# Optimization experiments

Measured on AMD Instinct MI355X. Metric: run time of the kernel, lower is better.

## Reference

```python
import jax, jax.numpy as jnp
import numpy as np

B, N, DIM, HEADS, RED = 8, 1024, 768, 12, 2
CR = DIM // RED  # 384 reduced channel dim
HD = CR // HEADS  # 32 head dim
EPS = 1e-5


def layer_norm(x, g, b):
    mu = jnp.mean(x, axis=-1, keepdims=True)
    var = jnp.var(x, axis=-1, keepdims=True)
    return (x - mu) * jax.lax.rsqrt(var + EPS) * g + b


def setup_inputs() -> dict:
    key = jax.random.key(0)
    ks = jax.random.split(key, 8)
    s_in = 1.0 / np.sqrt(DIM)
    s_cr = 1.0 / np.sqrt(CR)
    return {
        "x": jax.random.normal(ks[0], (B, N, DIM), dtype=jnp.float32),
        "ln0_g": jnp.ones((DIM,), jnp.float32),
        "ln0_b": jnp.zeros((DIM,), jnp.float32),
        "w_proj": jax.random.normal(ks[1], (CR, DIM), jnp.float32) * s_in,  # conv1x1 -> linear
        "b_proj": jnp.zeros((CR,), jnp.float32),
        "ln1_g": jnp.ones((CR,), jnp.float32),
        "ln1_b": jnp.zeros((CR,), jnp.float32),
        "wq": jax.random.normal(ks[2], (CR, CR), jnp.float32) * s_cr,
        "wk": jax.random.normal(ks[3], (CR, CR), jnp.float32) * s_cr,
        "wv": jax.random.normal(ks[4], (CR, CR), jnp.float32) * s_cr,
    }


def attention(y, wq, wk, wv):
    # y: [B, N, CR]; 1x1 conv == linear on channel dim
    def heads(w):
        return (y @ w.T).reshape(B, N, HEADS, HD).transpose(0, 2, 1, 3)  # [B,H,N,D]
    q, k, v = heads(wq), heads(wk), heads(wv)
    scale = HD ** -0.5
    attn = jax.nn.softmax(jnp.einsum("bhnd,bhmd->bhnm", q, k) * scale, axis=-1)
    out = jnp.einsum("bhnm,bhmd->bhnd", attn, v)  # [B,H,N,D]
    return out.transpose(0, 2, 1, 3).reshape(B, N, CR)


def reference(x, ln0_g, ln0_b, w_proj, b_proj, ln1_g, ln1_b, wq, wk, wv):
    h = layer_norm(x, ln0_g, ln0_b) @ w_proj.T + b_proj  # [B,N,CR]
    y = layer_norm(h, ln1_g, ln1_b)
    return h + attention(y, wq, wk, wv)
```

## Files before the change

kernel.cpp:

```cpp
#include <hip/hip_runtime.h>
#include <math.h>

#define BB 8
#define NN 1024
#define DIM 768
#define HEADS 12
#define CR 384
#define HD 32
#define MROWS (BB*NN)
#define EPS 1e-5f
#define SCALE_Q 0.25503486f

typedef __attribute__((ext_vector_type(8))) __bf16 bf16x8;
typedef __attribute__((ext_vector_type(8))) unsigned short u16x8;
typedef __attribute__((ext_vector_type(4))) float f32x4;

__device__ __forceinline__ unsigned short f2bf(float f) {
    unsigned int u = __float_as_uint(f);
    u += 0x7fffu + ((u >> 16) & 1u);
    return (unsigned short)(u >> 16);
}

__device__ __forceinline__ unsigned int packbf2(float lo, float hi) {
    return (unsigned int)f2bf(lo) | ((unsigned int)f2bf(hi) << 16);
}

__device__ __forceinline__ void async_cp16(const unsigned short* g, unsigned short* l) {
    __builtin_amdgcn_global_load_lds(
        (const __attribute__((address_space(1))) unsigned int*)g,
        (__attribute__((address_space(3))) unsigned int*)l, 16, 0, 0);
}

__global__ __launch_bounds__(256) void ln0_cast(
    const float* __restrict__ x,
    const float* __restrict__ g, const float* __restrict__ bt,
    unsigned short* __restrict__ a0,
    const float* __restrict__ wp, const float* __restrict__ wq,
    const float* __restrict__ wk, const float* __restrict__ wv,
    unsigned short* __restrict__ wpo, unsigned short* __restrict__ wqkvo)
{
    const int bx = blockIdx.x;
    const int t = threadIdx.x;
    if (bx >= MROWS) {
        int i = (bx - MROWS) * 256 + t;
        const float* src; unsigned short* dst; int off;
        if (i < 73728) { src = wp; dst = wpo; off = i; }
        else {
            int j = i - 73728;
            int sel = j / 36864; off = j % 36864;
            src = sel == 0 ? wq : (sel == 1 ? wk : wv);
            dst = wqkvo + (size_t)sel * 147456;
        }
        float4 v = ((const float4*)src)[off];
        ((ushort4*)dst)[off] = make_ushort4(f2bf(v.x), f2bf(v.y), f2bf(v.z), f2bf(v.w));
        return;
    }
    const int nv = DIM >> 2;
    const float* a = x + (size_t)bx * DIM;
    float4 val = make_float4(0.f, 0.f, 0.f, 0.f);
    float s = 0.f, ss = 0.f;
    if (t < nv) {
        val = ((const float4*)a)[t];
        s = val.x + val.y + val.z + val.w;
        ss = val.x * val.x + val.y * val.y + val.z * val.z + val.w * val.w;
    }
    for (int off = 32; off; off >>= 1) {
        s  += __shfl_down(s, off, 64);
        ss += __shfl_down(ss, off, 64);
    }
    __shared__ float rS[4], rSS[4];
    __shared__ float sh_mu, sh_rs;
    int lane = t & 63, w = t >> 6;
    if (lane == 0) { rS[w] = s; rSS[w] = ss; }
    __syncthreads();
    if (t == 0) {
        float S = rS[0] + rS[1] + rS[2] + rS[3];
        float SS = rSS[0] + rSS[1] + rSS[2] + rSS[3];
        float m = S / DIM;
        sh_mu = m;
        sh_rs = rsqrtf(SS / DIM - m * m + EPS);
    }
    __syncthreads();
    if (t < nv) {
        float m = sh_mu, r = sh_rs;
        float4 gv = ((const float4*)g)[t];
        float4 bv = ((const float4*)bt)[t];
        ((ushort4*)(a0 + (size_t)bx * DIM))[t] = make_ushort4(
            f2bf((val.x - m) * r * gv.x + bv.x),
            f2bf((val.y - m) * r * gv.y + bv.y),
            f2bf((val.z - m) * r * gv.z + bv.z),
            f2bf((val.w - m) * r * gv.w + bv.w));
    }
}

__global__ __launch_bounds__(128) void ln1_sum(
    const float* __restrict__ h0, const float* __restrict__ h1,
    const float* __restrict__ bias,
    const float* __restrict__ g, const float* __restrict__ bt,
    float* __restrict__ hs, unsigned short* __restrict__ y)
{
    const int row = blockIdx.x;
    const int t = threadIdx.x;
    const int nv = CR >> 2;
    float4 val = make_float4(0.f, 0.f, 0.f, 0.f);
    float s = 0.f, ss = 0.f;
    if (t < nv) {
        float4 v0 = ((const float4*)(h0 + (size_t)row * CR))[t];
        float4 v1 = ((const float4*)(h1 + (size_t)row * CR))[t];
        float4 bv = ((const float4*)bias)[t];
        val = make_float4(v0.x + v1.x + bv.x, v0.y + v1.y + bv.y,
                          v0.z + v1.z + bv.z, v0.w + v1.w + bv.w);
        ((float4*)(hs + (size_t)row * CR))[t] = val;
        s = val.x + val.y + val.z + val.w;
        ss = val.x * val.x + val.y * val.y + val.z * val.z + val.w * val.w;
    }
    for (int off = 32; off; off >>= 1) {
        s  += __shfl_down(s, off, 64);
        ss += __shfl_down(ss, off, 64);
    }
    __shared__ float rS[2], rSS[2];
    __shared__ float sh_mu, sh_rs;
    int lane = t & 63, w = t >> 6;
    if (lane == 0) { rS[w] = s; rSS[w] = ss; }
    __syncthreads();
    if (t == 0) {
        float S = rS[0] + rS[1];
        float SS = rSS[0] + rSS[1];
        float m = S / CR;
        sh_mu = m;
        sh_rs = rsqrtf(SS / CR - m * m + EPS);
    }
    __syncthreads();
    if (t < nv) {
        float m = sh_mu, r = sh_rs;
        float4 gv = ((const float4*)g)[t];
        float4 bv = ((const float4*)bt)[t];
        ((ushort4*)(y + (size_t)row * CR))[t] = make_ushort4(
            f2bf((val.x - m) * r * gv.x + bv.x),
            f2bf((val.y - m) * r * gv.y + bv.y),
            f2bf((val.z - m) * r * gv.z + bv.z),
            f2bf((val.w - m) * r * gv.w + bv.w));
    }
}

template<int KD, int NITER, int MODE>
__global__ __launch_bounds__(256) void gemm_mfma(
    const unsigned short* __restrict__ A,
    const unsigned short* __restrict__ W,
    void* __restrict__ C0, void* __restrict__ C1)
{
    __shared__ unsigned short Asm[2 * 128 * 32];
    __shared__ unsigned short Bsm[2 * 128 * 32];
    const int t = threadIdx.x;
    const int wave = t >> 6, lane = t & 63;
    const int l15 = lane & 15, quad = lane >> 4;
    const int m0 = blockIdx.y * 128;
    const int n0 = blockIdx.x * 128;
    const int koff = blockIdx.z * (NITER * 32);
    const int wm = (wave & 1) * 64, wn = (wave >> 1) * 64;

    const int srow = lane >> 2;
    const int skq  = (lane & 3) * 8;
    const unsigned short* gA = A + (size_t)(m0 + wave * 32 + srow) * KD + koff + skq;
    const unsigned short* gB = W + (size_t)(n0 + wave * 32 + srow) * KD + koff + skq;
    unsigned short* lA = Asm + wave * 1024;
    unsigned short* lB = Bsm + wave * 1024;

    async_cp16(gA, lA);
    async_cp16(gA + (size_t)16 * KD, lA + 512);
    async_cp16(gB, lB);
    async_cp16(gB + (size_t)16 * KD, lB + 512);

    f32x4 acc[4][4];
#pragma unroll
    for (int i = 0; i < 4; i++)
#pragma unroll
        for (int j = 0; j < 4; j++) acc[i][j] = (f32x4){0.f, 0.f, 0.f, 0.f};

    for (int it = 0; it < NITER; it++) {
        __syncthreads();
        const int cur = it & 1;
        if (it + 1 < NITER) {
            const int noff = (cur ^ 1) * 4096;
            async_cp16(gA + (it + 1) * 32, lA + noff);
            async_cp16(gA + (size_t)16 * KD + (it + 1) * 32, lA + noff + 512);
            async_cp16(gB + (it + 1) * 32, lB + noff);
            async_cp16(gB + (size_t)16 * KD + (it + 1) * 32, lB + noff + 512);
        }
        const unsigned short* Ab = Asm + cur * 4096;
        const unsigned short* Bb = Bsm + cur * 4096;
        bf16x8 af[4], bfr[4];
#pragma unroll
        for (int i = 0; i < 4; i++)
            af[i] = *(const bf16x8*)(Ab + (wm + i * 16 + l15) * 32 + quad * 8);
#pragma unroll
        for (int j = 0; j < 4; j++)
            bfr[j] = *(const bf16x8*)(Bb + (wn + j * 16 + l15) * 32 + quad * 8);
#pragma unroll
        for (int i = 0; i < 4; i++)
#pragma unroll
            for (int j = 0; j < 4; j++)
                acc[i][j] = __builtin_amdgcn_mfma_f32_16x16x32_bf16(af[i], bfr[j], acc[i][j], 0, 0, 0);
    }

    if constexpr (MODE == 0) {
        float* C = (float*)C0 + (size_t)blockIdx.z * MROWS * CR;
#pragma unroll
        for (int i = 0; i < 4; i++)
#pragma unroll
            for (int j = 0; j < 4; j++)
#pragma unroll
                for (int reg = 0; reg < 4; reg++) {
                    int row = m0 + wm + i * 16 + quad * 4 + reg;
                    int col = n0 + wn + j * 16 + l15;
                    C[(size_t)row * CR + col] = acc[i][j][reg];
                }
    } else {
        unsigned short* Cqk = (unsigned short*)C0;
        unsigned short* Vt  = (unsigned short*)C1;
#pragma unroll
        for (int i = 0; i < 4; i++)
#pragma unroll
            for (int j = 0; j < 4; j++) {
                const int colbase = n0 + wn + j * 16;
                const int token0 = m0 + wm + i * 16 + quad * 4;
                if (colbase < DIM) {
                    const float sc = (colbase < CR) ? SCALE_Q : 1.f;
#pragma unroll
                    for (int reg = 0; reg < 4; reg++)
                        Cqk[(size_t)(token0 + reg) * DIM + colbase + l15] = f2bf(acc[i][j][reg] * sc);
                } else {
                    const int ch = colbase - DIM + l15;
                    uint2 pk;
                    pk.x = packbf2(acc[i][j][0], acc[i][j][1]);
                    pk.y = packbf2(acc[i][j][2], acc[i][j][3]);
                    *(uint2*)(Vt + (size_t)ch * MROWS + token0) = pk;
                }
            }
    }
}

__global__ __launch_bounds__(256) void attn_mfma(
    const unsigned short* __restrict__ qk,
    const unsigned short* __restrict__ vt,
    const float* __restrict__ h, float* __restrict__ out)
{
    const int qt = blockIdx.x;
    const int bh = blockIdx.y;
    const int b = bh / HEADS, head = bh % HEADS;
    const int hc = head * HD;
    const int t = threadIdx.x;
    const int wave = t >> 6, lane = t & 63;
    const int l15 = lane & 15, quad = lane >> 4;
    const int q0 = qt * 128;

    __shared__ unsigned short Ks[64 * 40];
    __shared__ unsigned short Vs[32 * 72];
    __shared__ unsigned short Ps[4][32 * 72];
    unsigned short* Pw = Ps[wave];

    bf16x8 qa[2];
#pragma unroll
    for (int qi = 0; qi < 2; qi++)
        qa[qi] = *(const bf16x8*)(qk + (size_t)(b * NN + q0 + wave * 32 + qi * 16 + l15) * DIM
                                  + hc + quad * 8);

    const int rr = t >> 2, seg = t & 3;
    const unsigned short* gK = qk + (size_t)(b * NN + rr) * DIM + CR + hc + seg * 8;
    const int vch = wave * 8 + (lane >> 3), vko = (lane & 7) * 8;
    const unsigned short* gV = vt + (size_t)(hc + vch) * MROWS + b * NN + vko;

    u16x8 kreg = *(const u16x8*)gK;
    u16x8 vreg = *(const u16x8*)gV;

    f32x4 o[2][2] = {{{0.f,0.f,0.f,0.f},{0.f,0.f,0.f,0.f}},
                     {{0.f,0.f,0.f,0.f},{0.f,0.f,0.f,0.f}}};
    float lpart[2] = {0.f, 0.f};

    for (int kt = 0; kt < 16; kt++) {
        __syncthreads();
        *(u16x8*)(Ks + rr * 40 + seg * 8) = kreg;
        *(u16x8*)(Vs + vch * 72 + vko) = vreg;
        if (kt < 15) {
            kreg = *(const u16x8*)(gK + (size_t)(kt + 1) * 64 * DIM);
            vreg = *(const u16x8*)(gV + (kt + 1) * 64);
        }
        __syncthreads();

        bf16x8 kb[4];
#pragma unroll
        for (int nt = 0; nt < 4; nt++)
            kb[nt] = *(const bf16x8*)(Ks + (nt * 16 + l15) * 40 + quad * 8);

#pragma unroll
        for (int qi = 0; qi < 2; qi++) {
            f32x4 s[4];
#pragma unroll
            for (int nt = 0; nt < 4; nt++) {
                f32x4 z = {0.f, 0.f, 0.f, 0.f};
                s[nt] = __builtin_amdgcn_mfma_f32_16x16x32_bf16(kb[nt], qa[qi], z, 0, 0, 0);
            }
#pragma unroll
            for (int nt = 0; nt < 4; nt++) {
                float e0 = __builtin_amdgcn_exp2f(s[nt][0]);
                float e1 = __builtin_amdgcn_exp2f(s[nt][1]);
                float e2 = __builtin_amdgcn_exp2f(s[nt][2]);
                float e3 = __builtin_amdgcn_exp2f(s[nt][3]);
                lpart[qi] += (e0 + e1) + (e2 + e3);
                uint2 pk;
                pk.x = packbf2(e0, e1);
                pk.y = packbf2(e2, e3);
                *(uint2*)(Pw + (qi * 16 + l15) * 72 + nt * 16 + quad * 4) = pk;
            }
        }

        bf16x8 vb[2][2];
#pragma unroll
        for (int kk = 0; kk < 2; kk++)
#pragma unroll
            for (int nt2 = 0; nt2 < 2; nt2++)
                vb[kk][nt2] = *(const bf16x8*)(Vs + (nt2 * 16 + l15) * 72 + kk * 32 + quad * 8);

#pragma unroll
        for (int qi = 0; qi < 2; qi++)
#pragma unroll
            for (int kk = 0; kk < 2; kk++) {
                bf16x8 pa = *(const bf16x8*)(Pw + (qi * 16 + l15) * 72 + kk * 32 + quad * 8);
#pragma unroll
                for (int nt2 = 0; nt2 < 2; nt2++)
                    o[qi][nt2] = __builtin_amdgcn_mfma_f32_16x16x32_bf16(pa, vb[kk][nt2], o[qi][nt2], 0, 0, 0);
            }
    }

#pragma unroll
    for (int qi = 0; qi < 2; qi++) {
        float l = lpart[qi];
        l += __shfl_xor(l, 16, 64);
        l += __shfl_xor(l, 32, 64);
        const float linv = 1.f / l;
#pragma unroll
        for (int reg = 0; reg < 4; reg++) {
            const float li = __shfl(linv, quad * 4 + reg, 64);
            const size_t row = (size_t)(b * NN + q0 + wave * 32 + qi * 16 + quad * 4 + reg);
#pragma unroll
            for (int nt2 = 0; nt2 < 2; nt2++) {
                size_t idx = row * CR + hc + nt2 * 16 + l15;
                out[idx] = h[idx] + o[qi][nt2][reg] * li;
            }
        }
    }
}

extern "C" void kernel_launch(void* const* d_in, const int* in_sizes, int n_in,
                              void* d_out, int out_size, void* d_ws, size_t ws_size,
                              hipStream_t stream) {
    const float* x      = (const float*)d_in[0];
    const float* ln0_g  = (const float*)d_in[1];
    const float* ln0_b  = (const float*)d_in[2];
    const float* w_proj = (const float*)d_in[3];
    const float* b_proj = (const float*)d_in[4];
    const float* ln1_g  = (const float*)d_in[5];
    const float* ln1_b  = (const float*)d_in[6];
    const float* wq     = (const float*)d_in[7];
    const float* wk     = (const float*)d_in[8];
    const float* wv     = (const float*)d_in[9];
    float* out = (float*)d_out;

    char* base = (char*)d_ws;
    unsigned short* a0   = (unsigned short*)base;
    unsigned short* qkb  = (unsigned short*)base;
    float*          hp   = (float*)(base + 12582912);
    float*          hbuf = (float*)(base + 37748736);
    unsigned short* yb   = (unsigned short*)(base + 50331648);
    unsigned short* vtb  = (unsigned short*)(base + 56623104);
    unsigned short* wp   = (unsigned short*)(base + 62914560);
    unsigned short* wqkv = (unsigned short*)(base + 63504384);

    ln0_cast<<<MROWS + 720, 256, 0, stream>>>(x, ln0_g, ln0_b, a0,
                                              w_proj, wq, wk, wv, wp, wqkv);
    gemm_mfma<DIM, 12, 0><<<dim3(CR / 128, MROWS / 128, 2), 256, 0, stream>>>(
        a0, wp, hp, nullptr);
    ln1_sum<<<MROWS, 128, 0, stream>>>(hp, hp + (size_t)MROWS * CR, b_proj,
                                       ln1_g, ln1_b, hbuf, yb);
    gemm_mfma<CR, 12, 1><<<dim3(1152 / 128, MROWS / 128, 1), 256, 0, stream>>>(
        yb, wqkv, qkb, vtb);
    attn_mfma<<<dim3(NN / 128, BB * HEADS), 256, 0, stream>>>(qkb, vtb, hbuf, out);
}
```

Measured before the change: 165.3 us.

## Fuse all stages into one persistent cooperative kernel with grid syncs

Replaces the five separate kernel launches with a single persistent cooperative kernel that loops over row, GEMM-tile and attention-tile jobs. Stages are separated by grid-wide barriers instead of kernel boundaries, and the layer norms use one wave per row with shuffle reductions instead of a block per row. The aim is to remove launch gaps and tail effects between stages. In exchange, work is limited to the resident block count (at most 512), grid.sync has its own cost, and the launch falls back to separate kernels if the cooperative launch fails.

```diff
diff --git a/kernel.cpp b/kernel.cpp
--- a/kernel.cpp
+++ b/kernel.cpp
@@ -1,5 +1,9 @@
 #include <hip/hip_runtime.h>
+#include <hip/hip_bf16.h>
+#include <hip/hip_cooperative_groups.h>
 #include <math.h>
+
+namespace cg = cooperative_groups;
 
 #define BB 8
 #define NN 1024
@@ -22,7 +26,9 @@
 }
 
 __device__ __forceinline__ unsigned int packbf2(float lo, float hi) {
-    return (unsigned int)f2bf(lo) | ((unsigned int)f2bf(hi) << 16);
+    __hip_bfloat162 h2 = __float22bfloat162_rn(make_float2(lo, hi));
+    unsigned int u; __builtin_memcpy(&u, &h2, sizeof(u));
+    return u;
 }
 
 __device__ __forceinline__ void async_cp16(const unsigned short* g, unsigned short* l) {
@@ -31,11 +37,351 @@
         (__attribute__((address_space(3))) unsigned int*)l, 16, 0, 0);
 }
 
-__global__ __launch_bounds__(256) void ln0_cast(
+
+template<int KD, int NITER, int MODE>
+__device__ void gemm_tile(const unsigned short* __restrict__ A,
+                          const unsigned short* __restrict__ W,
+                          int m0, int n0, int koff,
+                          unsigned short* Asm, unsigned short* Bsm,
+                          void* C0, void* C1)
+{
+    const int t = threadIdx.x;
+    const int wave = t >> 6, lane = t & 63;
+    const int l15 = lane & 15, quad = lane >> 4;
+    const int wm = (wave & 1) * 64, wn = (wave >> 1) * 64;
+    const int srow = lane >> 2;
+    const int skq  = (lane & 3) * 8;
+    const unsigned short* gA = A + (size_t)(m0 + wave * 32 + srow) * KD + koff + skq;
+    const unsigned short* gB = W + (size_t)(n0 + wave * 32 + srow) * KD + koff + skq;
+    unsigned short* lA = Asm + wave * 1024;
+    unsigned short* lB = Bsm + wave * 1024;
+
+    async_cp16(gA, lA);
+    async_cp16(gA + (size_t)16 * KD, lA + 512);
+    async_cp16(gB, lB);
+    async_cp16(gB + (size_t)16 * KD, lB + 512);
+
+    f32x4 acc[4][4];
+#pragma unroll
+    for (int i = 0; i < 4; i++)
+#pragma unroll
+        for (int j = 0; j < 4; j++) acc[i][j] = (f32x4){0.f, 0.f, 0.f, 0.f};
+
+    for (int it = 0; it < NITER; it++) {
+        __syncthreads();
+        const int cur = it & 1;
+        if (it + 1 < NITER) {
+            const int noff = (cur ^ 1) * 4096;
+            async_cp16(gA + (it + 1) * 32, lA + noff);
+            async_cp16(gA + (size_t)16 * KD + (it + 1) * 32, lA + noff + 512);
+            async_cp16(gB + (it + 1) * 32, lB + noff);
+            async_cp16(gB + (size_t)16 * KD + (it + 1) * 32, lB + noff + 512);
+        }
+        const unsigned short* Ab = Asm + cur * 4096;
+        const unsigned short* Bb = Bsm + cur * 4096;
+        bf16x8 af[4], bfr[4];
+#pragma unroll
+        for (int i = 0; i < 4; i++)
+            af[i] = *(const bf16x8*)(Ab + (wm + i * 16 + l15) * 32 + quad * 8);
+#pragma unroll
+        for (int j = 0; j < 4; j++)
+            bfr[j] = *(const bf16x8*)(Bb + (wn + j * 16 + l15) * 32 + quad * 8);
+#pragma unroll
+        for (int i = 0; i < 4; i++)
+#pragma unroll
+            for (int j = 0; j < 4; j++)
+                acc[i][j] = __builtin_amdgcn_mfma_f32_16x16x32_bf16(af[i], bfr[j], acc[i][j], 0, 0, 0);
+    }
+    __syncthreads();
+
+    if constexpr (MODE == 0) {
+        float* C = (float*)C0;
+#pragma unroll
+        for (int i = 0; i < 4; i++)
+#pragma unroll
+            for (int j = 0; j < 4; j++)
+#pragma unroll
+                for (int reg = 0; reg < 4; reg++) {
+                    int row = m0 + wm + i * 16 + quad * 4 + reg;
+                    int col = n0 + wn + j * 16 + l15;
+                    C[(size_t)row * CR + col] = acc[i][j][reg];
+                }
+    } else {
+        unsigned short* Cqk = (unsigned short*)C0;
+        unsigned short* Vt  = (unsigned short*)C1;
+#pragma unroll
+        for (int i = 0; i < 4; i++)
+#pragma unroll
+            for (int j = 0; j < 4; j++) {
+                const int colbase = n0 + wn + j * 16;
+                const int token0 = m0 + wm + i * 16 + quad * 4;
+                if (colbase < DIM) {
+                    const float sc = (colbase < CR) ? SCALE_Q : 1.f;
+#pragma unroll
+                    for (int reg = 0; reg < 4; reg++)
+                        Cqk[(size_t)(token0 + reg) * DIM + colbase + l15] = f2bf(acc[i][j][reg] * sc);
+                } else {
+                    const int ch = colbase - DIM + l15;
+                    uint2 pk;
+                    pk.x = packbf2(acc[i][j][0], acc[i][j][1]);
+                    pk.y = packbf2(acc[i][j][2], acc[i][j][3]);
+                    *(uint2*)(Vt + (size_t)ch * MROWS + token0) = pk;
+                }
+            }
+    }
+}
+
+__device__ void attn_tile(int qt, int bh,
+                          const unsigned short* __restrict__ qk,
+                          const unsigned short* __restrict__ vt,
+                          const float* __restrict__ h, float* __restrict__ out,
+                          unsigned short* Ks, unsigned short* Vs, unsigned short* PsBase)
+{
+    const int b = bh / HEADS, head = bh % HEADS;
+    const int hc = head * HD;
+    const int t = threadIdx.x;
+    const int wave = t >> 6, lane = t & 63;
+    const int l15 = lane & 15, quad = lane >> 4;
+    const int q0 = qt * 128;
+    unsigned short* Pw = PsBase + wave * (32 * 72);
+
+    bf16x8 qa[2];
+#pragma unroll
+    for (int qi = 0; qi < 2; qi++)
+        qa[qi] = *(const bf16x8*)(qk + (size_t)(b * NN + q0 + wave * 32 + qi * 16 + l15) * DIM
+                                  + hc + quad * 8);
+
+    const int rr = t >> 2, seg = t & 3;
+    const unsigned short* gK = qk + (size_t)(b * NN + rr) * DIM + CR + hc + seg * 8;
+    const int vch = wave * 8 + (lane >> 3), vko = (lane & 7) * 8;
+    const unsigned short* gV = vt + (size_t)(hc + vch) * MROWS + b * NN + vko;
+
+    u16x8 kreg = *(const u16x8*)gK;
+    u16x8 vreg = *(const u16x8*)gV;
+
+    f32x4 o[2][2] = {{{0.f,0.f,0.f,0.f},{0.f,0.f,0.f,0.f}},
+                     {{0.f,0.f,0.f,0.f},{0.f,0.f,0.f,0.f}}};
+    float lpart[2] = {0.f, 0.f};
+
+    for (int kt = 0; kt < 16; kt++) {
+        __syncthreads();
+        *(u16x8*)(Ks + rr * 40 + seg * 8) = kreg;
+        *(u16x8*)(Vs + vch * 72 + vko) = vreg;
+        if (kt < 15) {
+            kreg = *(const u16x8*)(gK + (size_t)(kt + 1) * 64 * DIM);
+            vreg = *(const u16x8*)(gV + (kt + 1) * 64);
+        }
+        __syncthreads();
+
+        bf16x8 kb[4];
+#pragma unroll
+        for (int nt = 0; nt < 4; nt++)
+            kb[nt] = *(const bf16x8*)(Ks + (nt * 16 + l15) * 40 + quad * 8);
+
+#pragma unroll
+        for (int qi = 0; qi < 2; qi++) {
+            f32x4 s[4];
+#pragma unroll
+            for (int nt = 0; nt < 4; nt++) {
+                f32x4 z = {0.f, 0.f, 0.f, 0.f};
+                s[nt] = __builtin_amdgcn_mfma_f32_16x16x32_bf16(kb[nt], qa[qi], z, 0, 0, 0);
+            }
+#pragma unroll
+            for (int nt = 0; nt < 4; nt++) {
+                float e0 = __builtin_amdgcn_exp2f(s[nt][0]);
+                float e1 = __builtin_amdgcn_exp2f(s[nt][1]);
+                float e2 = __builtin_amdgcn_exp2f(s[nt][2]);
+                float e3 = __builtin_amdgcn_exp2f(s[nt][3]);
+                lpart[qi] += (e0 + e1) + (e2 + e3);
+                uint2 pk;
+                pk.x = packbf2(e0, e1);
+                pk.y = packbf2(e2, e3);
+                *(uint2*)(Pw + (qi * 16 + l15) * 72 + nt * 16 + quad * 4) = pk;
+            }
+        }
+
+        bf16x8 vb[2][2];
+#pragma unroll
+        for (int kk = 0; kk < 2; kk++)
+#pragma unroll
+            for (int nt2 = 0; nt2 < 2; nt2++)
+                vb[kk][nt2] = *(const bf16x8*)(Vs + (nt2 * 16 + l15) * 72 + kk * 32 + quad * 8);
+
+#pragma unroll
+        for (int qi = 0; qi < 2; qi++)
+#pragma unroll
+            for (int kk = 0; kk < 2; kk++) {
+                bf16x8 pa = *(const bf16x8*)(Pw + (qi * 16 + l15) * 72 + kk * 32 + quad * 8);
+#pragma unroll
+                for (int nt2 = 0; nt2 < 2; nt2++)
+                    o[qi][nt2] = __builtin_amdgcn_mfma_f32_16x16x32_bf16(pa, vb[kk][nt2], o[qi][nt2], 0, 0, 0);
+            }
+    }
+    __syncthreads();
+
+#pragma unroll
+    for (int qi = 0; qi < 2; qi++) {
+        float l = lpart[qi];
+        l += __shfl_xor(l, 16, 64);
+        l += __shfl_xor(l, 32, 64);
+        const float linv = 1.f / l;
+#pragma unroll
+        for (int reg = 0; reg < 4; reg++) {
+            const float li = __shfl(linv, quad * 4 + reg, 64);
+            const size_t row = (size_t)(b * NN + q0 + wave * 32 + qi * 16 + quad * 4 + reg);
+#pragma unroll
+            for (int nt2 = 0; nt2 < 2; nt2++) {
+                size_t idx = row * CR + hc + nt2 * 16 + l15;
+                out[idx] = h[idx] + o[qi][nt2][reg] * li;
+            }
+        }
+    }
+}
+
+union Smem {
+    struct { unsigned short A[2 * 128 * 32]; unsigned short B[2 * 128 * 32]; } g;
+    struct { unsigned short Ks[64 * 40]; unsigned short Vs[32 * 72];
+             unsigned short Ps[4 * 32 * 72]; } at;
+};
+
+__global__ __launch_bounds__(256, 2) void fused_all(
+    const float* __restrict__ x,
+    const float* __restrict__ ln0_g, const float* __restrict__ ln0_b,
+    const float* __restrict__ w_proj, const float* __restrict__ b_proj,
+    const float* __restrict__ ln1_g, const float* __restrict__ ln1_b,
+    const float* __restrict__ wq, const float* __restrict__ wk,
+    const float* __restrict__ wv,
+    unsigned short* a0, unsigned short* wp, unsigned short* wqkv,
+    float* hp, float* hbuf, unsigned short* yb,
+    unsigned short* qkb, unsigned short* vtb, float* out, int nblk)
+{
+    __shared__ Smem sm;
+    cg::grid_group grid = cg::this_grid();
+    const int bid = blockIdx.x;
+    const int t = threadIdx.x;
+    const int wave = t >> 6, lane = t & 63;
+
+#pragma unroll 1
+    for (int row = bid * 4 + wave; row < MROWS; row += nblk * 4) {
+        const float* a = x + (size_t)row * DIM;
+        float4 v[3]; float s = 0.f, ss = 0.f;
+#pragma unroll
+        for (int c = 0; c < 3; c++) {
+            v[c] = ((const float4*)a)[lane + c * 64];
+            s  += v[c].x + v[c].y + v[c].z + v[c].w;
+            ss += v[c].x * v[c].x + v[c].y * v[c].y + v[c].z * v[c].z + v[c].w * v[c].w;
+        }
+#pragma unroll
+        for (int off = 1; off < 64; off <<= 1) {
+            s += __shfl_xor(s, off, 64); ss += __shfl_xor(ss, off, 64);
+        }
+        const float mu = s / DIM, rs = rsqrtf(ss / DIM - mu * mu + EPS);
+#pragma unroll
+        for (int c = 0; c < 3; c++) {
+            float4 gv = ((const float4*)ln0_g)[lane + c * 64];
+            float4 bv = ((const float4*)ln0_b)[lane + c * 64];
+            uint2 pk;
+            pk.x = packbf2((v[c].x - mu) * rs * gv.x + bv.x, (v[c].y - mu) * rs * gv.y + bv.y);
+            pk.y = packbf2((v[c].z - mu) * rs * gv.z + bv.z, (v[c].w - mu) * rs * gv.w + bv.w);
+            *(uint2*)(a0 + (size_t)row * DIM + (lane + c * 64) * 4) = pk;
+        }
+    }
+#pragma unroll 1
+    for (int i = bid * 256 + t; i < 184320; i += nblk * 256) {
+        const float* src; unsigned short* dst; int off;
+        if (i < 73728) { src = w_proj; dst = wp; off = i; }
+        else {
+            int j = i - 73728;
+            int sel = j / 36864; off = j % 36864;
+            src = sel == 0 ? wq : (sel == 1 ? wk : wv);
+            dst = wqkv + (size_t)sel * 147456;
+        }
+        float4 v = ((const float4*)src)[off];
+        uint2 pk; pk.x = packbf2(v.x, v.y); pk.y = packbf2(v.z, v.w);
+        ((uint2*)dst)[off] = pk;
+    }
+    __threadfence(); grid.sync();
+
+#pragma unroll 1
+    for (int job = bid; job < 384; job += nblk) {
+        const int n0 = (job % 3) * 128;
+        const int m0 = ((job / 3) & 63) * 128;
+        const int z  = job / 192;
+        gemm_tile<DIM, 12, 0>(a0, wp, m0, n0, z * 384, sm.g.A, sm.g.B,
+                              hp + (size_t)z * MROWS * CR, nullptr);
+    }
+    __threadfence(); grid.sync();
+
+    {
+        const float* h1 = hp + (size_t)MROWS * CR;
+#pragma unroll 1
+        for (int row = bid * 4 + wave; row < MROWS; row += nblk * 4) {
+            float4 c0 = make_float4(0.f,0.f,0.f,0.f), c1 = make_float4(0.f,0.f,0.f,0.f);
+            float s = 0.f, ss = 0.f;
+            {
+                float4 p = ((const float4*)(hp + (size_t)row * CR))[lane];
+                float4 q = ((const float4*)(h1 + (size_t)row * CR))[lane];
+                float4 b = ((const float4*)b_proj)[lane];
+                c0 = make_float4(p.x + q.x + b.x, p.y + q.y + b.y,
+                                 p.z + q.z + b.z, p.w + q.w + b.w);
+                s  += c0.x + c0.y + c0.z + c0.w;
+                ss += c0.x * c0.x + c0.y * c0.y + c0.z * c0.z + c0.w * c0.w;
+            }
+            if (lane < 32) {
+                float4 p = ((const float4*)(hp + (size_t)row * CR))[64 + lane];
+                float4 q = ((const float4*)(h1 + (size_t)row * CR))[64 + lane];
+                float4 b = ((const float4*)b_proj)[64 + lane];
+                c1 = make_float4(p.x + q.x + b.x, p.y + q.y + b.y,
+                                 p.z + q.z + b.z, p.w + q.w + b.w);
+                s  += c1.x + c1.y + c1.z + c1.w;
+                ss += c1.x * c1.x + c1.y * c1.y + c1.z * c1.z + c1.w * c1.w;
+            }
+#pragma unroll
+            for (int off = 1; off < 64; off <<= 1) {
+                s += __shfl_xor(s, off, 64); ss += __shfl_xor(ss, off, 64);
+            }
+            const float mu = s / CR, rs = rsqrtf(ss / CR - mu * mu + EPS);
+            {
+                ((float4*)(hbuf + (size_t)row * CR))[lane] = c0;
+                float4 gv = ((const float4*)ln1_g)[lane];
+                float4 bv = ((const float4*)ln1_b)[lane];
+                uint2 pk;
+                pk.x = packbf2((c0.x - mu) * rs * gv.x + bv.x, (c0.y - mu) * rs * gv.y + bv.y);
+                pk.y = packbf2((c0.z - mu) * rs * gv.z + bv.z, (c0.w - mu) * rs * gv.w + bv.w);
+                *(uint2*)(yb + (size_t)row * CR + lane * 4) = pk;
+            }
+            if (lane < 32) {
+                ((float4*)(hbuf + (size_t)row * CR))[64 + lane] = c1;
+                float4 gv = ((const float4*)ln1_g)[64 + lane];
+                float4 bv = ((const float4*)ln1_b)[64 + lane];
+                uint2 pk;
+                pk.x = packbf2((c1.x - mu) * rs * gv.x + bv.x, (c1.y - mu) * rs * gv.y + bv.y);
+                pk.y = packbf2((c1.z - mu) * rs * gv.z + bv.z, (c1.w - mu) * rs * gv.w + bv.w);
+                *(uint2*)(yb + (size_t)row * CR + (64 + lane) * 4) = pk;
+            }
+        }
+    }
+    __threadfence(); grid.sync();
+
+#pragma unroll 1
+    for (int job = bid; job < 576; job += nblk) {
+        const int n0 = (job % 9) * 128;
+        const int m0 = (job / 9) * 128;
+        gemm_tile<CR, 12, 1>(yb, wqkv, m0, n0, 0, sm.g.A, sm.g.B, qkb, vtb);
+    }
+    __threadfence(); grid.sync();
+
+#pragma unroll 1
+    for (int job = bid; job < 768; job += nblk)
+        attn_tile(job & 7, job >> 3, qkb, vtb, hbuf, out, sm.at.Ks, sm.at.Vs, sm.at.Ps);
+}
+
+
+__global__ __launch_bounds__(256) void ln0_cast_k(
     const float* __restrict__ x,
     const float* __restrict__ g, const float* __restrict__ bt,
     unsigned short* __restrict__ a0,
-    const float* __restrict__ wp, const float* __restrict__ wq,
+    const float* __restrict__ wpf, const float* __restrict__ wq,
     const float* __restrict__ wk, const float* __restrict__ wv,
     unsigned short* __restrict__ wpo, unsigned short* __restrict__ wqkvo)
 {
@@ -44,7 +390,7 @@
     if (bx >= MROWS) {
         int i = (bx - MROWS) * 256 + t;
         const float* src; unsigned short* dst; int off;
-        if (i < 73728) { src = wp; dst = wpo; off = i; }
+        if (i < 73728) { src = wpf; dst = wpo; off = i; }
         else {
             int j = i - 73728;
             int sel = j / 36864; off = j % 36864;
@@ -93,7 +439,7 @@
     }
 }
 
-__global__ __launch_bounds__(128) void ln1_sum(
+__global__ __launch_bounds__(128) void ln1_sum_k(
     const float* __restrict__ h0, const float* __restrict__ h1,
     const float* __restrict__ bias,
     const float* __restrict__ g, const float* __restrict__ bt,
@@ -144,211 +490,28 @@
 }
 
 template<int KD, int NITER, int MODE>
-__global__ __launch_bounds__(256) void gemm_mfma(
+__global__ __launch_bounds__(256) void gemm_mfma_k(
     const unsigned short* __restrict__ A,
     const unsigned short* __restrict__ W,
     void* __restrict__ C0, void* __restrict__ C1)
 {
     __shared__ unsigned short Asm[2 * 128 * 32];
     __shared__ unsigned short Bsm[2 * 128 * 32];
-    const int t = threadIdx.x;
-    const int wave = t >> 6, lane = t & 63;
-    const int l15 = lane & 15, quad = lane >> 4;
     const int m0 = blockIdx.y * 128;
     const int n0 = blockIdx.x * 128;
     const int koff = blockIdx.z * (NITER * 32);
-    const int wm = (wave & 1) * 64, wn = (wave >> 1) * 64;
-
-    const int srow = lane >> 2;
-    const int skq  = (lane & 3) * 8;
-    const unsigned short* gA = A + (size_t)(m0 + wave * 32 + srow) * KD + koff + skq;
-    const unsigned short* gB = W + (size_t)(n0 + wave * 32 + srow) * KD + koff + skq;
-    unsigned short* lA = Asm + wave * 1024;
-    unsigned short* lB = Bsm + wave * 1024;
-
-    async_cp16(gA, lA);
-    async_cp16(gA + (size_t)16 * KD, lA + 512);
-    async_cp16(gB, lB);
-    async_cp16(gB + (size_t)16 * KD, lB + 512);
-
-    f32x4 acc[4][4];
-#pragma unroll
-    for (int i = 0; i < 4; i++)
-#pragma unroll
-        for (int j = 0; j < 4; j++) acc[i][j] = (f32x4){0.f, 0.f, 0.f, 0.f};
-
-    for (int it = 0; it < NITER; it++) {
-        __syncthreads();
-        const int cur = it & 1;
-        if (it + 1 < NITER) {
-            const int noff = (cur ^ 1) * 4096;
-            async_cp16(gA + (it + 1) * 32, lA + noff);
-            async_cp16(gA + (size_t)16 * KD + (it + 1) * 32, lA + noff + 512);
-            async_cp16(gB + (it + 1) * 32, lB + noff);
-            async_cp16(gB + (size_t)16 * KD + (it + 1) * 32, lB + noff + 512);
-        }
-        const unsigned short* Ab = Asm + cur * 4096;
-        const unsigned short* Bb = Bsm + cur * 4096;
-        bf16x8 af[4], bfr[4];
-#pragma unroll
-        for (int i = 0; i < 4; i++)
-            af[i] = *(const bf16x8*)(Ab + (wm + i * 16 + l15) * 32 + quad * 8);
-#pragma unroll
-        for (int j = 0; j < 4; j++)
-            bfr[j] = *(const bf16x8*)(Bb + (wn + j * 16 + l15) * 32 + quad * 8);
-#pragma unroll
-        for (int i = 0; i < 4; i++)
-#pragma unroll
-            for (int j = 0; j < 4; j++)
-                acc[i][j] = __builtin_amdgcn_mfma_f32_16x16x32_bf16(af[i], bfr[j], acc[i][j], 0, 0, 0);
-    }
-
-    if constexpr (MODE == 0) {
-        float* C = (float*)C0 + (size_t)blockIdx.z * MROWS * CR;
-#pragma unroll
-        for (int i = 0; i < 4; i++)
-#pragma unroll
-            for (int j = 0; j < 4; j++)
-#pragma unroll
-                for (int reg = 0; reg < 4; reg++) {
-                    int row = m0 + wm + i * 16 + quad * 4 + reg;
-                    int col = n0 + wn + j * 16 + l15;
-                    C[(size_t)row * CR + col] = acc[i][j][reg];
-                }
-    } else {
-        unsigned short* Cqk = (unsigned short*)C0;
-        unsigned short* Vt  = (unsigned short*)C1;
-#pragma unroll
-        for (int i = 0; i < 4; i++)
-#pragma unroll
-            for (int j = 0; j < 4; j++) {
-                const int colbase = n0 + wn + j * 16;
-                const int token0 = m0 + wm + i * 16 + quad * 4;
-                if (colbase < DIM) {
-                    const float sc = (colbase < CR) ? SCALE_Q : 1.f;
-#pragma unroll
-                    for (int reg = 0; reg < 4; reg++)
-                        Cqk[(size_t)(token0 + reg) * DIM + colbase + l15] = f2bf(acc[i][j][reg] * sc);
-                } else {
-                    const int ch = colbase - DIM + l15;
-                    uint2 pk;
-                    pk.x = packbf2(acc[i][j][0], acc[i][j][1]);
-                    pk.y = packbf2(acc[i][j][2], acc[i][j][3]);
-                    *(uint2*)(Vt + (size_t)ch * MROWS + token0) = pk;
-                }
-            }
-    }
-}
-
-__global__ __launch_bounds__(256) void attn_mfma(
-    const unsigned short* __restrict__ qk,
-    const unsigned short* __restrict__ vt,
+    void* C0z = (MODE == 0) ? (void*)((float*)C0 + (size_t)blockIdx.z * MROWS * CR) : C0;
+    gemm_tile<KD, NITER, MODE>(A, W, m0, n0, koff, Asm, Bsm, C0z, C1);
+}
+
+__global__ __launch_bounds__(256) void attn_mfma_k(
+    const unsigned short* __restrict__ qk, const unsigned short* __restrict__ vt,
     const float* __restrict__ h, float* __restrict__ out)
 {
-    const int qt = blockIdx.x;
-    const int bh = blockIdx.y;
-    const int b = bh / HEADS, head = bh % HEADS;
-    const int hc = head * HD;
-    const int t = threadIdx.x;
-    const int wave = t >> 6, lane = t & 63;
-    const int l15 = lane & 15, quad = lane >> 4;
-    const int q0 = qt * 128;
-
     __shared__ unsigned short Ks[64 * 40];
     __shared__ unsigned short Vs[32 * 72];
-    __shared__ unsigned short Ps[4][32 * 72];
-    unsigned short* Pw = Ps[wave];
-
-    bf16x8 qa[2];
-#pragma unroll
-    for (int qi = 0; qi < 2; qi++)
-        qa[qi] = *(const bf16x8*)(qk + (size_t)(b * NN + q0 + wave * 32 + qi * 16 + l15) * DIM
-                                  + hc + quad * 8);
-
-    const int rr = t >> 2, seg = t & 3;
-    const unsigned short* gK = qk + (size_t)(b * NN + rr) * DIM + CR + hc + seg * 8;
-    const int vch = wave * 8 + (lane >> 3), vko = (lane & 7) * 8;
-    const unsigned short* gV = vt + (size_t)(hc + vch) * MROWS + b * NN + vko;
-
-    u16x8 kreg = *(const u16x8*)gK;
-    u16x8 vreg = *(const u16x8*)gV;
-
-    f32x4 o[2][2] = {{{0.f,0.f,0.f,0.f},{0.f,0.f,0.f,0.f}},
-                     {{0.f,0.f,0.f,0.f},{0.f,0.f,0.f,0.f}}};
-    float lpart[2] = {0.f, 0.f};
-
-    for (int kt = 0; kt < 16; kt++) {
-        __syncthreads();
-        *(u16x8*)(Ks + rr * 40 + seg * 8) = kreg;
-        *(u16x8*)(Vs + vch * 72 + vko) = vreg;
-        if (kt < 15) {
-            kreg = *(const u16x8*)(gK + (size_t)(kt + 1) * 64 * DIM);
-            vreg = *(const u16x8*)(gV + (kt + 1) * 64);
-        }
-        __syncthreads();
-
-        bf16x8 kb[4];
-#pragma unroll
-        for (int nt = 0; nt < 4; nt++)
-            kb[nt] = *(const bf16x8*)(Ks + (nt * 16 + l15) * 40 + quad * 8);
-
-#pragma unroll
-        for (int qi = 0; qi < 2; qi++) {
-            f32x4 s[4];
-#pragma unroll
-            for (int nt = 0; nt < 4; nt++) {
-                f32x4 z = {0.f, 0.f, 0.f, 0.f};
-                s[nt] = __builtin_amdgcn_mfma_f32_16x16x32_bf16(kb[nt], qa[qi], z, 0, 0, 0);
-            }
-#pragma unroll
-            for (int nt = 0; nt < 4; nt++) {
-                float e0 = __builtin_amdgcn_exp2f(s[nt][0]);
-                float e1 = __builtin_amdgcn_exp2f(s[nt][1]);
-                float e2 = __builtin_amdgcn_exp2f(s[nt][2]);
-                float e3 = __builtin_amdgcn_exp2f(s[nt][3]);
-                lpart[qi] += (e0 + e1) + (e2 + e3);
-                uint2 pk;
-                pk.x = packbf2(e0, e1);
-                pk.y = packbf2(e2, e3);
-                *(uint2*)(Pw + (qi * 16 + l15) * 72 + nt * 16 + quad * 4) = pk;
-            }
-        }
-
-        bf16x8 vb[2][2];
-#pragma unroll
-        for (int kk = 0; kk < 2; kk++)
-#pragma unroll
-            for (int nt2 = 0; nt2 < 2; nt2++)
-                vb[kk][nt2] = *(const bf16x8*)(Vs + (nt2 * 16 + l15) * 72 + kk * 32 + quad * 8);
-
-#pragma unroll
-        for (int qi = 0; qi < 2; qi++)
-#pragma unroll
-            for (int kk = 0; kk < 2; kk++) {
-                bf16x8 pa = *(const bf16x8*)(Pw + (qi * 16 + l15) * 72 + kk * 32 + quad * 8);
-#pragma unroll
-                for (int nt2 = 0; nt2 < 2; nt2++)
-                    o[qi][nt2] = __builtin_amdgcn_mfma_f32_16x16x32_bf16(pa, vb[kk][nt2], o[qi][nt2], 0, 0, 0);
-            }
-    }
-
-#pragma unroll
-    for (int qi = 0; qi < 2; qi++) {
-        float l = lpart[qi];
-        l += __shfl_xor(l, 16, 64);
-        l += __shfl_xor(l, 32, 64);
-        const float linv = 1.f / l;
-#pragma unroll
-        for (int reg = 0; reg < 4; reg++) {
-            const float li = __shfl(linv, quad * 4 + reg, 64);
-            const size_t row = (size_t)(b * NN + q0 + wave * 32 + qi * 16 + quad * 4 + reg);
-#pragma unroll
-            for (int nt2 = 0; nt2 < 2; nt2++) {
-                size_t idx = row * CR + hc + nt2 * 16 + l15;
-                out[idx] = h[idx] + o[qi][nt2][reg] * li;
-            }
-        }
-    }
+    __shared__ unsigned short Ps[4 * 32 * 72];
+    attn_tile(blockIdx.x, blockIdx.y, qk, vt, h, out, Ks, Vs, Ps);
 }
 
 extern "C" void kernel_launch(void* const* d_in, const int* in_sizes, int n_in,
@@ -376,13 +539,29 @@
     unsigned short* wp   = (unsigned short*)(base + 62914560);
     unsigned short* wqkv = (unsigned short*)(base + 63504384);
 
-    ln0_cast<<<MROWS + 720, 256, 0, stream>>>(x, ln0_g, ln0_b, a0,
-                                              w_proj, wq, wk, wv, wp, wqkv);
-    gemm_mfma<DIM, 12, 0><<<dim3(CR / 128, MROWS / 128, 2), 256, 0, stream>>>(
-        a0, wp, hp, nullptr);
-    ln1_sum<<<MROWS, 128, 0, stream>>>(hp, hp + (size_t)MROWS * CR, b_proj,
-                                       ln1_g, ln1_b, hbuf, yb);
-    gemm_mfma<CR, 12, 1><<<dim3(1152 / 128, MROWS / 128, 1), 256, 0, stream>>>(
-        yb, wqkv, qkb, vtb);
-    attn_mfma<<<dim3(NN / 128, BB * HEADS), 256, 0, stream>>>(qkb, vtb, hbuf, out);
-}
+    int maxb = 0;
+    hipError_t occ = hipOccupancyMaxActiveBlocksPerMultiprocessor(&maxb, fused_all, 256, 0);
+    int nblk = 256;
+    if (occ == hipSuccess && maxb >= 1) {
+        nblk = maxb * 256;
+        if (nblk > 512) nblk = 512;
+    }
+
+    void* args[] = { (void*)&x, (void*)&ln0_g, (void*)&ln0_b, (void*)&w_proj, (void*)&b_proj,
+                     (void*)&ln1_g, (void*)&ln1_b, (void*)&wq, (void*)&wk, (void*)&wv,
+                     (void*)&a0, (void*)&wp, (void*)&wqkv, (void*)&hp, (void*)&hbuf,
+                     (void*)&yb, (void*)&qkb, (void*)&vtb, (void*)&out, (void*)&nblk };
+    hipError_t e = hipLaunchCooperativeKernel((void*)fused_all, dim3(nblk), dim3(256),
+                                              args, 0, stream);
+    if (e != hipSuccess) {
+        ln0_cast_k<<<MROWS + 720, 256, 0, stream>>>(x, ln0_g, ln0_b, a0,
+                                                    w_proj, wq, wk, wv, wp, wqkv);
+        gemm_mfma_k<DIM, 12, 0><<<dim3(CR / 128, MROWS / 128, 2), 256, 0, stream>>>(
+            a0, wp, hp, nullptr);
+        ln1_sum_k<<<MROWS, 128, 0, stream>>>(hp, hp + (size_t)MROWS * CR, b_proj,
+                                             ln1_g, ln1_b, hbuf, yb);
+        gemm_mfma_k<CR, 12, 1><<<dim3(1152 / 128, MROWS / 128, 1), 256, 0, stream>>>(
+            yb, wqkv, qkb, vtb);
+        attn_mfma_k<<<dim3(NN / 128, BB * HEADS), 256, 0, stream>>>(qkb, vtb, hbuf, out);
+    }
+}
```

After: 446.2 us. +170.0%, slower.
